# Kernel tuning notes

Measured on AMD Instinct MI355X. Metric: run time of the kernel, lower is better.

## Reference

```python
import jax, jax.numpy as jnp
import numpy as np

BS, SEQ, D = 8, 2048, 128
MASK_VALUE = -1000000.0


def setup_inputs() -> dict:
    key = jax.random.key(0)
    kq, kk, kv, kl = jax.random.split(key, 4)
    return {
        "queries": jax.random.normal(kq, (BS, SEQ, D), dtype=jnp.float32),
        "keys": jax.random.normal(kk, (BS, SEQ, D), dtype=jnp.float32),
        "values": jax.random.normal(kv, (BS, SEQ, D), dtype=jnp.float32),
        "valid_lens": jax.random.randint(kl, (BS,), 1, SEQ + 1, dtype=jnp.int32),
    }


def reference(queries, keys, values, valid_lens):
    d_k = keys.shape[-1]
    # (bs, seq_q, seq_k)
    scores = jnp.einsum("bqd,bkd->bqk", queries, keys) / jnp.sqrt(
        jnp.asarray(d_k, dtype=queries.dtype)
    )
    # padding mask over the LAST axis: position k valid iff k < valid_len[b]
    pos = jnp.arange(scores.shape[-1])  # (seq_k,)
    valid = pos[None, None, :] < valid_lens[:, None, None]  # (bs, 1, seq_k)
    scores = jnp.where(valid, scores, MASK_VALUE)
    attn = jax.nn.softmax(scores, axis=-1)
    # (bs, seq_q, d_v); dropout=0.0 -> identity
    return jnp.einsum("bqk,bkd->bqd", attn, values)
```

## Files before the change

### kernel.cpp

```cpp
#include <hip/hip_runtime.h>

typedef float f32x4 __attribute__((ext_vector_type(4)));
typedef short bf16x8 __attribute__((ext_vector_type(8)));
typedef short bf16x4 __attribute__((ext_vector_type(4)));
typedef unsigned int u32x2 __attribute__((ext_vector_type(2)));

#define BS    8
#define SEQ   2048
#define DH    128
#define BQ    32
#define BK    64
#define NT    256
#define CFIX  8.0f
#define SC2E  0.12751743f
#define NC2E  -11.541560327f

__device__ __forceinline__ unsigned short f2bf(float x) {
    unsigned u = __float_as_uint(x);
    u += 0x7FFFu + ((u >> 16) & 1u);
    return (unsigned short)(u >> 16);
}

__device__ __forceinline__ void gl_lds16(const unsigned short* g, unsigned short* l) {
    __builtin_amdgcn_global_load_lds(
        (const __attribute__((address_space(1))) unsigned int*)g,
        (__attribute__((address_space(3))) unsigned int*)l, 16, 0, 0);
}

__global__ __launch_bounds__(NT)
void conv_all(const float* __restrict__ K, const float* __restrict__ V,
              unsigned short* __restrict__ Kbf, unsigned short* __restrict__ Vt) {
    __shared__ unsigned short T[64][132];
    const int tid = threadIdx.x;
    const int bid = blockIdx.x;

    const int gtid = bid * NT + tid;
    #pragma unroll
    for (int i = 0; i < 8; ++i) {
        const int idx = i * (256 * NT) + gtid;
        float4 v = ((const float4*)K)[idx];
        ushort4 h;
        h.x = f2bf(v.x); h.y = f2bf(v.y); h.z = f2bf(v.z); h.w = f2bf(v.w);
        ((ushort4*)Kbf)[idx] = h;
    }

    const int vb = bid >> 5, s0 = (bid & 31) * 64;
    const float* Vb = V + ((size_t)vb * SEQ + s0) * DH;
    #pragma unroll
    for (int i = 0; i < 8; ++i) {
        const int row = i * 8 + (tid >> 5);
        const int col = (tid & 31) * 4;
        float4 v = *(const float4*)(Vb + (size_t)row * DH + col);
        ushort4 h;
        h.x = f2bf(v.x); h.y = f2bf(v.y); h.z = f2bf(v.z); h.w = f2bf(v.w);
        *(ushort4*)&T[row][col] = h;
    }
    __syncthreads();
    const int d = tid >> 1, sh = (tid & 1) * 32;
    unsigned short tmp[32] __attribute__((aligned(16)));
    #pragma unroll
    for (int s = 0; s < 32; ++s) tmp[s] = T[sh + s][d];
    unsigned short* dst = Vt + ((size_t)vb * DH + d) * SEQ + s0 + sh;
    #pragma unroll
    for (int g = 0; g < 4; ++g)
        *(uint4*)(dst + g * 8) = *(const uint4*)(tmp + g * 8);
}

__global__ __launch_bounds__(NT, 2)
void attn32(const float* __restrict__ Q, const unsigned short* __restrict__ Kbf,
            const unsigned short* __restrict__ Vt, const int* __restrict__ vlens,
            float* __restrict__ Out) {
    __shared__ unsigned short Ks[2][BK * DH];
    __shared__ unsigned short Vs[2][DH * BK];
    __shared__ float Lsc[2][32];

    const int tid  = threadIdx.x;
    const int wid  = tid >> 6, lane = tid & 63;
    const int quad = lane >> 4, l16 = lane & 15;
    const int qh   = wid >> 1, sh = wid & 1;
    const int bid  = blockIdx.x;
    const int b    = bid >> 6;
    const int q0   = (bid & 63) * BQ;
    const int vl   = vlens[b];

    const unsigned short* Kb  = Kbf + (size_t)b * SEQ * DH;
    const unsigned short* Vtb = Vt  + (size_t)b * DH * SEQ;

    bf16x8 qf[4];
    {
        const float* Qr = Q + ((size_t)b * SEQ + q0 + 16 * qh + l16) * DH;
        #pragma unroll
        for (int ks = 0; ks < 4; ++ks) {
            const float4 x = *(const float4*)(Qr + 32 * ks + 8 * quad);
            const float4 y = *(const float4*)(Qr + 32 * ks + 8 * quad + 4);
            unsigned short t8[8] __attribute__((aligned(16)));
            t8[0] = f2bf(x.x); t8[1] = f2bf(x.y); t8[2] = f2bf(x.z); t8[3] = f2bf(x.w);
            t8[4] = f2bf(y.x); t8[5] = f2bf(y.y); t8[6] = f2bf(y.z); t8[7] = f2bf(y.w);
            qf[ks] = *(const bf16x8*)t8;
        }
    }

    f32x4 o[8];
    #pragma unroll
    for (int n = 0; n < 8; ++n) o[n] = (f32x4){0.f, 0.f, 0.f, 0.f};
    float lsum = 0.f;

    const int ntiles = (vl + BK - 1) >> 6;

    auto stage = [&](int buf, int k0) {
        unsigned short* KsB = &Ks[buf][0];
        unsigned short* VsB = &Vs[buf][0];
        #pragma unroll
        for (int ii = 0; ii < 4; ++ii) {
            const int rb = 16 * wid + 4 * ii;
            const int r  = rb + (lane >> 4);
            const int c  = lane & 15;
            gl_lds16(Kb + (size_t)(k0 + r) * DH + ((c ^ (r & 15)) << 3),
                     KsB + (size_t)rb * DH);
        }
        #pragma unroll
        for (int jj = 0; jj < 4; ++jj) {
            const int db = 32 * wid + 8 * jj;
            const int d  = db + (lane >> 3);
            const int c  = lane & 7;
            gl_lds16(Vtb + (size_t)d * SEQ + k0 + ((c ^ (d & 7)) << 3),
                     VsB + (size_t)db * BK);
        }
    };

    stage(0, 0);

    for (int t = 0; t < ntiles; ++t) {
        const int k0 = t << 6;
        __syncthreads();
        if (t + 1 < ntiles) stage((t + 1) & 1, k0 + BK);

        const unsigned short* Kt  = &Ks[t & 1][0];
        const unsigned short* Vtl = &Vs[t & 1][0];

        f32x4 s2[2];
        s2[0] = (f32x4){0.f, 0.f, 0.f, 0.f};
        s2[1] = (f32x4){0.f, 0.f, 0.f, 0.f};
        __builtin_amdgcn_s_setprio(1);
        #pragma unroll
        for (int ks = 0; ks < 4; ++ks) {
            bf16x8 bk[2];
            #pragma unroll
            for (int nt = 0; nt < 2; ++nt)
                bk[nt] = *(const bf16x8*)(Kt + (size_t)(32 * sh + 16 * nt + l16) * DH +
                                          (((4 * ks + quad) ^ l16) << 3));
            #pragma unroll
            for (int nt = 0; nt < 2; ++nt)
                s2[nt] = __builtin_amdgcn_mfma_f32_16x16x32_bf16(bk[nt], qf[ks], s2[nt], 0, 0, 0);
        }
        __builtin_amdgcn_s_setprio(0);

        float p[2][4];
        if (k0 + BK <= vl) {
            #pragma unroll
            for (int nt = 0; nt < 2; ++nt)
                #pragma unroll
                for (int r = 0; r < 4; ++r) {
                    const float pv = __builtin_amdgcn_exp2f(fmaf(s2[nt][r], SC2E, NC2E));
                    p[nt][r] = pv;
                    lsum += pv;
                }
        } else {
            const int kb = k0 + 32 * sh + 4 * quad;
            #pragma unroll
            for (int nt = 0; nt < 2; ++nt)
                #pragma unroll
                for (int r = 0; r < 4; ++r) {
                    float pv = __builtin_amdgcn_exp2f(fmaf(s2[nt][r], SC2E, NC2E));
                    pv = (kb + 16 * nt + r < vl) ? pv : 0.0f;
                    p[nt][r] = pv;
                    lsum += pv;
                }
        }

        bf16x4 pa[2];
        #pragma unroll
        for (int nt = 0; nt < 2; ++nt) {
            unsigned w0, w1;
            asm("v_cvt_pk_bf16_f32 %0, %1, %2" : "=v"(w0) : "v"(p[nt][0]), "v"(p[nt][1]));
            asm("v_cvt_pk_bf16_f32 %0, %1, %2" : "=v"(w1) : "v"(p[nt][2]), "v"(p[nt][3]));
            u32x2 tw; tw.x = w0; tw.y = w1;
            pa[nt] = __builtin_bit_cast(bf16x4, tw);
        }

        __builtin_amdgcn_s_setprio(1);
        #pragma unroll
        for (int n = 0; n < 8; ++n) {
            const int dd = 16 * n + l16;
            #pragma unroll
            for (int nt = 0; nt < 2; ++nt) {
                const int g = 4 * sh + 2 * nt + (quad >> 1);
                const bf16x4 vb = *(const bf16x4*)(Vtl + (size_t)dd * BK +
                                        ((g ^ (dd & 7)) << 3) + ((quad & 1) << 2));
                o[n] = __builtin_amdgcn_mfma_f32_16x16x16bf16_1k(pa[nt], vb, o[n], 0, 0, 0);
            }
        }
        __builtin_amdgcn_s_setprio(0);
    }

    lsum += __shfl_xor(lsum, 16, 64);
    lsum += __shfl_xor(lsum, 32, 64);

    __syncthreads();
    float* Osc = (float*)&Ks[0][0];

    if (lane < 16) Lsc[sh][qh * 16 + l16] = lsum;
    if (sh == 0) {
        #pragma unroll
        for (int r = 0; r < 4; ++r) {
            float* dst = Osc + (size_t)qh * 2048 + (4 * quad + r) * 128 + l16;
            #pragma unroll
            for (int n = 0; n < 8; ++n) dst[16 * n] = o[n][r];
        }
    }
    __syncthreads();
    if (sh == 1) {
        #pragma unroll
        for (int r = 0; r < 4; ++r) {
            const float ls = Lsc[0][qh * 16 + 4 * quad + r] +
                             Lsc[1][qh * 16 + 4 * quad + r];
            const float inv = 1.0f / ls;
            const float* src = Osc + (size_t)qh * 2048 + (4 * quad + r) * 128 + l16;
            float* Or = Out + ((size_t)b * SEQ + q0 + 16 * qh + 4 * quad + r) * DH + l16;
            #pragma unroll
            for (int n = 0; n < 8; ++n)
                Or[16 * n] = (o[n][r] + src[16 * n]) * inv;
        }
    }
}

#define FBQ 32
#define QSTRIDE (DH + 4)
#define PSTRIDE (BK + 4)
__global__ __launch_bounds__(NT, 2)
void attn_fwd(const float* __restrict__ Q, const float* __restrict__ K,
              const float* __restrict__ V, const int* __restrict__ vlens,
              float* __restrict__ Out) {
    __shared__ float Qs[FBQ][QSTRIDE];
    __shared__ float KVs[BK][QSTRIDE];
    __shared__ float Ps[FBQ][PSTRIDE];
    __shared__ float l_s[FBQ];
    const int tid = threadIdx.x;
    const int b = blockIdx.y, q0 = blockIdx.x * FBQ;
    const int vl = vlens[b];
    const float scale = 0.088388347648318441f;
    const float* Qb = Q + ((size_t)b * SEQ + q0) * DH;
    const float* Kb = K + (size_t)b * SEQ * DH;
    const float* Vb = V + (size_t)b * SEQ * DH;
    {
        const int r = tid >> 5, c4 = (tid & 31) * 4;
        #pragma unroll
        for (int i = 0; i < 4; ++i)
            *(float4*)&Qs[i * 8 + r][c4] = *(const float4*)(Qb + (size_t)(i * 8 + r) * DH + c4);
    }
    const int sty = tid >> 4, stx = tid & 15;
    const int brow = tid >> 3, bpart = tid & 7;
    const int prg = tid >> 5, pcg = tid & 31;
    float lacc = 0.0f;
    float O[4][4];
    #pragma unroll
    for (int i = 0; i < 4; ++i)
        #pragma unroll
        for (int j = 0; j < 4; ++j) O[i][j] = 0.0f;
    const int ntiles = (vl + BK - 1) / BK;
    for (int t = 0; t < ntiles; ++t) {
        const int k0 = t * BK;
        __syncthreads();
        {
            const int r = tid >> 5, c4 = (tid & 31) * 4;
            #pragma unroll
            for (int i = 0; i < 8; ++i)
                *(float4*)&KVs[i * 8 + r][c4] = *(const float4*)(Kb + (size_t)(k0 + i * 8 + r) * DH + c4);
        }
        __syncthreads();
        float s0[4] = {0.f, 0.f, 0.f, 0.f}, s1[4] = {0.f, 0.f, 0.f, 0.f};
        #pragma unroll 2
        for (int d = 0; d < DH; d += 4) {
            const float4 qa = *(const float4*)&Qs[2 * sty][d];
            const float4 qb = *(const float4*)&Qs[2 * sty + 1][d];
            #pragma unroll
            for (int j = 0; j < 4; ++j) {
                const float4 kk = *(const float4*)&KVs[4 * stx + j][d];
                s0[j] += qa.x * kk.x + qa.y * kk.y + qa.z * kk.z + qa.w * kk.w;
                s1[j] += qb.x * kk.x + qb.y * kk.y + qb.z * kk.z + qb.w * kk.w;
            }
        }
        #pragma unroll
        for (int j = 0; j < 4; ++j) {
            const int kk = k0 + 4 * stx + j;
            const bool valid = kk < vl;
            Ps[2 * sty][4 * stx + j]     = valid ? __expf(s0[j] * scale - CFIX) : 0.f;
            Ps[2 * sty + 1][4 * stx + j] = valid ? __expf(s1[j] * scale - CFIX) : 0.f;
        }
        __syncthreads();
        {
            float ps = 0.f;
            #pragma unroll
            for (int i = 0; i < 8; ++i) ps += Ps[brow][bpart * 8 + i];
            #pragma unroll
            for (int off = 1; off < 8; off <<= 1) ps += __shfl_xor(ps, off, 64);
            if (bpart == 0) lacc += ps;
        }
        {
            const int r = tid >> 5, c4 = (tid & 31) * 4;
            float4 vreg[8];
            #pragma unroll
            for (int i = 0; i < 8; ++i)
                vreg[i] = *(const float4*)(Vb + (size_t)(k0 + i * 8 + r) * DH + c4);
            __syncthreads();
            #pragma unroll
            for (int i = 0; i < 8; ++i) *(float4*)&KVs[i * 8 + r][c4] = vreg[i];
        }
        __syncthreads();
        for (int k = 0; k < BK; k += 4) {
            float4 pr[4];
            #pragma unroll
            for (int i = 0; i < 4; ++i) pr[i] = *(const float4*)&Ps[prg * 4 + i][k];
            #pragma unroll
            for (int k2 = 0; k2 < 4; ++k2) {
                const float4 vv = *(const float4*)&KVs[k + k2][pcg * 4];
                #pragma unroll
                for (int i = 0; i < 4; ++i) {
                    const float p = ((const float*)&pr[i])[k2];
                    O[i][0] += p * vv.x; O[i][1] += p * vv.y;
                    O[i][2] += p * vv.z; O[i][3] += p * vv.w;
                }
            }
        }
    }
    if (bpart == 0) l_s[brow] = lacc;
    __syncthreads();
    float* Ob = Out + ((size_t)b * SEQ + q0) * DH;
    #pragma unroll
    for (int i = 0; i < 4; ++i) {
        const int row = prg * 4 + i;
        const float inv = 1.0f / l_s[row];
        float4 ov;
        ov.x = O[i][0] * inv; ov.y = O[i][1] * inv;
        ov.z = O[i][2] * inv; ov.w = O[i][3] * inv;
        *(float4*)(Ob + (size_t)row * DH + pcg * 4) = ov;
    }
}

extern "C" void kernel_launch(void* const* d_in, const int* in_sizes, int n_in,
                              void* d_out, int out_size, void* d_ws, size_t ws_size,
                              hipStream_t stream) {
    const float* Q = (const float*)d_in[0];
    const float* K = (const float*)d_in[1];
    const float* V = (const float*)d_in[2];
    const int* vlens = (const int*)d_in[3];
    float* Out = (float*)d_out;

    const size_t n = (size_t)BS * SEQ * DH;
    const size_t need = 2 * n * 2;

    if (ws_size >= need) {
        unsigned short* Kbf = (unsigned short*)d_ws;
        unsigned short* Vt  = Kbf + n;
        conv_all<<<dim3(256), dim3(NT), 0, stream>>>(K, V, Kbf, Vt);
        attn32<<<dim3(BS * (SEQ / BQ)), dim3(NT), 0, stream>>>(Q, Kbf, Vt, vlens, Out);
    } else {
        attn_fwd<<<dim3(SEQ / FBQ, BS), dim3(NT), 0, stream>>>(Q, K, V, vlens, Out);
    }
}
```

Before: 110.3 us.

## Halve attention tiles to 16 queries, split head dim across waves, pre-convert Q

The attention kernel now uses 16-query, 32-key tiles, giving 1024 blocks instead of 512. The four waves are split two ways on key halves and two ways on head-dim halves. Q is converted to bf16 in the prep kernel, so the attention kernel loads bf16 fragments directly, and the occupancy hint rises to 4 blocks per CU. The goal is better load balance and occupancy across CUs with variable valid lengths. The cost is twice as many K/V tile loads per query, smaller MFMA work per barrier, and an extra Q conversion pass through memory.

```diff
diff --git a/kernel.cpp b/kernel.cpp
--- a/kernel.cpp
+++ b/kernel.cpp
@@ -8,8 +8,8 @@
 #define BS    8
 #define SEQ   2048
 #define DH    128
-#define BQ    32
-#define BK    64
+#define BQ    16
+#define BK    32
 #define NT    256
 #define CFIX  8.0f
 #define SC2E  0.12751743f
@@ -28,8 +28,10 @@
 }
 
 __global__ __launch_bounds__(NT)
-void conv_all(const float* __restrict__ K, const float* __restrict__ V,
-              unsigned short* __restrict__ Kbf, unsigned short* __restrict__ Vt) {
+void conv_all(const float* __restrict__ Q, const float* __restrict__ K,
+              const float* __restrict__ V,
+              unsigned short* __restrict__ Qbf, unsigned short* __restrict__ Kbf,
+              unsigned short* __restrict__ Vt) {
     __shared__ unsigned short T[64][132];
     const int tid = threadIdx.x;
     const int bid = blockIdx.x;
@@ -38,10 +40,13 @@
     #pragma unroll
     for (int i = 0; i < 8; ++i) {
         const int idx = i * (256 * NT) + gtid;
-        float4 v = ((const float4*)K)[idx];
-        ushort4 h;
-        h.x = f2bf(v.x); h.y = f2bf(v.y); h.z = f2bf(v.z); h.w = f2bf(v.w);
-        ((ushort4*)Kbf)[idx] = h;
+        float4 k4 = ((const float4*)K)[idx];
+        float4 q4 = ((const float4*)Q)[idx];
+        ushort4 hk, hq;
+        hk.x = f2bf(k4.x); hk.y = f2bf(k4.y); hk.z = f2bf(k4.z); hk.w = f2bf(k4.w);
+        hq.x = f2bf(q4.x); hq.y = f2bf(q4.y); hq.z = f2bf(q4.z); hq.w = f2bf(q4.w);
+        ((ushort4*)Kbf)[idx] = hk;
+        ((ushort4*)Qbf)[idx] = hq;
     }
 
     const int vb = bid >> 5, s0 = (bid & 31) * 64;
@@ -66,21 +71,21 @@
         *(uint4*)(dst + g * 8) = *(const uint4*)(tmp + g * 8);
 }
 
-__global__ __launch_bounds__(NT, 2)
-void attn32(const float* __restrict__ Q, const unsigned short* __restrict__ Kbf,
+__global__ __launch_bounds__(NT, 4)
+void attn16(const unsigned short* __restrict__ Qbf, const unsigned short* __restrict__ Kbf,
             const unsigned short* __restrict__ Vt, const int* __restrict__ vlens,
             float* __restrict__ Out) {
     __shared__ unsigned short Ks[2][BK * DH];
     __shared__ unsigned short Vs[2][DH * BK];
-    __shared__ float Lsc[2][32];
+    __shared__ float Lsc[2][16];
 
     const int tid  = threadIdx.x;
     const int wid  = tid >> 6, lane = tid & 63;
     const int quad = lane >> 4, l16 = lane & 15;
-    const int qh   = wid >> 1, sh = wid & 1;
+    const int dh   = wid >> 1, sh = wid & 1;
     const int bid  = blockIdx.x;
-    const int b    = bid >> 6;
-    const int q0   = (bid & 63) * BQ;
+    const int b    = bid >> 7;
+    const int q0   = (bid & 127) * BQ;
     const int vl   = vlens[b];
 
     const unsigned short* Kb  = Kbf + (size_t)b * SEQ * DH;
@@ -88,42 +93,36 @@
 
     bf16x8 qf[4];
     {
-        const float* Qr = Q + ((size_t)b * SEQ + q0 + 16 * qh + l16) * DH;
-        #pragma unroll
-        for (int ks = 0; ks < 4; ++ks) {
-            const float4 x = *(const float4*)(Qr + 32 * ks + 8 * quad);
-            const float4 y = *(const float4*)(Qr + 32 * ks + 8 * quad + 4);
-            unsigned short t8[8] __attribute__((aligned(16)));
-            t8[0] = f2bf(x.x); t8[1] = f2bf(x.y); t8[2] = f2bf(x.z); t8[3] = f2bf(x.w);
-            t8[4] = f2bf(y.x); t8[5] = f2bf(y.y); t8[6] = f2bf(y.z); t8[7] = f2bf(y.w);
-            qf[ks] = *(const bf16x8*)t8;
-        }
-    }
-
-    f32x4 o[8];
-    #pragma unroll
-    for (int n = 0; n < 8; ++n) o[n] = (f32x4){0.f, 0.f, 0.f, 0.f};
+        const unsigned short* Qr = Qbf + ((size_t)b * SEQ + q0 + l16) * DH;
+        #pragma unroll
+        for (int ks = 0; ks < 4; ++ks)
+            qf[ks] = *(const bf16x8*)(Qr + 32 * ks + 8 * quad);
+    }
+
+    f32x4 o[4];
+    #pragma unroll
+    for (int n = 0; n < 4; ++n) o[n] = (f32x4){0.f, 0.f, 0.f, 0.f};
     float lsum = 0.f;
 
-    const int ntiles = (vl + BK - 1) >> 6;
+    const int ntiles = (vl + BK - 1) >> 5;
 
     auto stage = [&](int buf, int k0) {
         unsigned short* KsB = &Ks[buf][0];
         unsigned short* VsB = &Vs[buf][0];
         #pragma unroll
-        for (int ii = 0; ii < 4; ++ii) {
-            const int rb = 16 * wid + 4 * ii;
+        for (int ii = 0; ii < 2; ++ii) {
+            const int rb = 8 * wid + 4 * ii;
             const int r  = rb + (lane >> 4);
             const int c  = lane & 15;
             gl_lds16(Kb + (size_t)(k0 + r) * DH + ((c ^ (r & 15)) << 3),
                      KsB + (size_t)rb * DH);
         }
         #pragma unroll
-        for (int jj = 0; jj < 4; ++jj) {
-            const int db = 32 * wid + 8 * jj;
-            const int d  = db + (lane >> 3);
-            const int c  = lane & 7;
-            gl_lds16(Vtb + (size_t)d * SEQ + k0 + ((c ^ (d & 7)) << 3),
+        for (int jj = 0; jj < 2; ++jj) {
+            const int db = 32 * wid + 16 * jj;
+            const int d  = db + (lane >> 2);
+            const int c  = lane & 3;
+            gl_lds16(Vtb + (size_t)d * SEQ + k0 + ((c ^ (d & 3)) << 3),
                      VsB + (size_t)db * BK);
         }
     };
@@ -131,74 +130,59 @@
     stage(0, 0);
 
     for (int t = 0; t < ntiles; ++t) {
-        const int k0 = t << 6;
+        const int k0 = t << 5;
         __syncthreads();
         if (t + 1 < ntiles) stage((t + 1) & 1, k0 + BK);
 
         const unsigned short* Kt  = &Ks[t & 1][0];
         const unsigned short* Vtl = &Vs[t & 1][0];
 
-        f32x4 s2[2];
-        s2[0] = (f32x4){0.f, 0.f, 0.f, 0.f};
-        s2[1] = (f32x4){0.f, 0.f, 0.f, 0.f};
+        f32x4 s2 = (f32x4){0.f, 0.f, 0.f, 0.f};
         __builtin_amdgcn_s_setprio(1);
         #pragma unroll
         for (int ks = 0; ks < 4; ++ks) {
-            bf16x8 bk[2];
-            #pragma unroll
-            for (int nt = 0; nt < 2; ++nt)
-                bk[nt] = *(const bf16x8*)(Kt + (size_t)(32 * sh + 16 * nt + l16) * DH +
-                                          (((4 * ks + quad) ^ l16) << 3));
-            #pragma unroll
-            for (int nt = 0; nt < 2; ++nt)
-                s2[nt] = __builtin_amdgcn_mfma_f32_16x16x32_bf16(bk[nt], qf[ks], s2[nt], 0, 0, 0);
+            const bf16x8 bk = *(const bf16x8*)(Kt + (size_t)(16 * sh + l16) * DH +
+                                               (((4 * ks + quad) ^ l16) << 3));
+            s2 = __builtin_amdgcn_mfma_f32_16x16x32_bf16(bk, qf[ks], s2, 0, 0, 0);
         }
         __builtin_amdgcn_s_setprio(0);
 
-        float p[2][4];
+        float p[4];
         if (k0 + BK <= vl) {
             #pragma unroll
-            for (int nt = 0; nt < 2; ++nt)
-                #pragma unroll
-                for (int r = 0; r < 4; ++r) {
-                    const float pv = __builtin_amdgcn_exp2f(fmaf(s2[nt][r], SC2E, NC2E));
-                    p[nt][r] = pv;
-                    lsum += pv;
-                }
+            for (int r = 0; r < 4; ++r) {
+                const float pv = __builtin_amdgcn_exp2f(fmaf(s2[r], SC2E, NC2E));
+                p[r] = pv;
+                lsum += pv;
+            }
         } else {
-            const int kb = k0 + 32 * sh + 4 * quad;
-            #pragma unroll
-            for (int nt = 0; nt < 2; ++nt)
-                #pragma unroll
-                for (int r = 0; r < 4; ++r) {
-                    float pv = __builtin_amdgcn_exp2f(fmaf(s2[nt][r], SC2E, NC2E));
-                    pv = (kb + 16 * nt + r < vl) ? pv : 0.0f;
-                    p[nt][r] = pv;
-                    lsum += pv;
-                }
-        }
-
-        bf16x4 pa[2];
-        #pragma unroll
-        for (int nt = 0; nt < 2; ++nt) {
+            const int kb = k0 + 16 * sh + 4 * quad;
+            #pragma unroll
+            for (int r = 0; r < 4; ++r) {
+                float pv = __builtin_amdgcn_exp2f(fmaf(s2[r], SC2E, NC2E));
+                pv = (kb + r < vl) ? pv : 0.0f;
+                p[r] = pv;
+                lsum += pv;
+            }
+        }
+
+        bf16x4 pa;
+        {
             unsigned w0, w1;
-            asm("v_cvt_pk_bf16_f32 %0, %1, %2" : "=v"(w0) : "v"(p[nt][0]), "v"(p[nt][1]));
-            asm("v_cvt_pk_bf16_f32 %0, %1, %2" : "=v"(w1) : "v"(p[nt][2]), "v"(p[nt][3]));
+            asm("v_cvt_pk_bf16_f32 %0, %1, %2" : "=v"(w0) : "v"(p[0]), "v"(p[1]));
+            asm("v_cvt_pk_bf16_f32 %0, %1, %2" : "=v"(w1) : "v"(p[2]), "v"(p[3]));
             u32x2 tw; tw.x = w0; tw.y = w1;
-            pa[nt] = __builtin_bit_cast(bf16x4, tw);
+            pa = __builtin_bit_cast(bf16x4, tw);
         }
 
         __builtin_amdgcn_s_setprio(1);
         #pragma unroll
-        for (int n = 0; n < 8; ++n) {
-            const int dd = 16 * n + l16;
-            #pragma unroll
-            for (int nt = 0; nt < 2; ++nt) {
-                const int g = 4 * sh + 2 * nt + (quad >> 1);
-                const bf16x4 vb = *(const bf16x4*)(Vtl + (size_t)dd * BK +
-                                        ((g ^ (dd & 7)) << 3) + ((quad & 1) << 2));
-                o[n] = __builtin_amdgcn_mfma_f32_16x16x16bf16_1k(pa[nt], vb, o[n], 0, 0, 0);
-            }
+        for (int n = 0; n < 4; ++n) {
+            const int d = 64 * dh + 16 * n + l16;
+            const int c = 2 * sh + (quad >> 1);
+            const bf16x4 vb = *(const bf16x4*)(Vtl + (size_t)d * BK +
+                                    ((c ^ (d & 3)) << 3) + ((quad & 1) << 2));
+            o[n] = __builtin_amdgcn_mfma_f32_16x16x16bf16_1k(pa, vb, o[n], 0, 0, 0);
         }
         __builtin_amdgcn_s_setprio(0);
     }
@@ -209,40 +193,41 @@
     __syncthreads();
     float* Osc = (float*)&Ks[0][0];
 
-    if (lane < 16) Lsc[sh][qh * 16 + l16] = lsum;
+    if (dh == 0 && lane < 16) Lsc[sh][l16] = lsum;
     if (sh == 0) {
         #pragma unroll
-        for (int r = 0; r < 4; ++r) {
-            float* dst = Osc + (size_t)qh * 2048 + (4 * quad + r) * 128 + l16;
-            #pragma unroll
-            for (int n = 0; n < 8; ++n) dst[16 * n] = o[n][r];
-        }
+        for (int n = 0; n < 4; ++n)
+            #pragma unroll
+            for (int r = 0; r < 4; ++r)
+                Osc[((size_t)dh * 16 + 4 * quad + r) * 64 + 16 * n + l16] = o[n][r];
     }
     __syncthreads();
     if (sh == 1) {
         #pragma unroll
         for (int r = 0; r < 4; ++r) {
-            const float ls = Lsc[0][qh * 16 + 4 * quad + r] +
-                             Lsc[1][qh * 16 + 4 * quad + r];
+            const int row = 4 * quad + r;
+            const float ls = Lsc[0][row] + Lsc[1][row];
             const float inv = 1.0f / ls;
-            const float* src = Osc + (size_t)qh * 2048 + (4 * quad + r) * 128 + l16;
-            float* Or = Out + ((size_t)b * SEQ + q0 + 16 * qh + 4 * quad + r) * DH + l16;
-            #pragma unroll
-            for (int n = 0; n < 8; ++n)
-                Or[16 * n] = (o[n][r] + src[16 * n]) * inv;
+            #pragma unroll
+            for (int n = 0; n < 4; ++n) {
+                const float val = (o[n][r] +
+                    Osc[((size_t)dh * 16 + row) * 64 + 16 * n + l16]) * inv;
+                Out[((size_t)b * SEQ + q0 + row) * DH + 64 * dh + 16 * n + l16] = val;
+            }
         }
     }
 }
 
 #define FBQ 32
+#define FBK 64
 #define QSTRIDE (DH + 4)
-#define PSTRIDE (BK + 4)
+#define PSTRIDE (FBK + 4)
 __global__ __launch_bounds__(NT, 2)
 void attn_fwd(const float* __restrict__ Q, const float* __restrict__ K,
               const float* __restrict__ V, const int* __restrict__ vlens,
               float* __restrict__ Out) {
     __shared__ float Qs[FBQ][QSTRIDE];
-    __shared__ float KVs[BK][QSTRIDE];
+    __shared__ float KVs[FBK][QSTRIDE];
     __shared__ float Ps[FBQ][PSTRIDE];
     __shared__ float l_s[FBQ];
     const int tid = threadIdx.x;
@@ -266,10 +251,10 @@
     #pragma unroll
     for (int i = 0; i < 4; ++i)
         #pragma unroll
-        for (int j = 0; j < 4; ++j) O[i][j] = 0.0f;
-    const int ntiles = (vl + BK - 1) / BK;
+        for (int jj = 0; jj < 4; ++jj) O[i][jj] = 0.0f;
+    const int ntiles = (vl + FBK - 1) / FBK;
     for (int t = 0; t < ntiles; ++t) {
-        const int k0 = t * BK;
+        const int k0 = t * FBK;
         __syncthreads();
         {
             const int r = tid >> 5, c4 = (tid & 31) * 4;
@@ -284,18 +269,18 @@
             const float4 qa = *(const float4*)&Qs[2 * sty][d];
             const float4 qb = *(const float4*)&Qs[2 * sty + 1][d];
             #pragma unroll
-            for (int j = 0; j < 4; ++j) {
-                const float4 kk = *(const float4*)&KVs[4 * stx + j][d];
-                s0[j] += qa.x * kk.x + qa.y * kk.y + qa.z * kk.z + qa.w * kk.w;
-                s1[j] += qb.x * kk.x + qb.y * kk.y + qb.z * kk.z + qb.w * kk.w;
-            }
-        }
-        #pragma unroll
-        for (int j = 0; j < 4; ++j) {
-            const int kk = k0 + 4 * stx + j;
+            for (int jj = 0; jj < 4; ++jj) {
+                const float4 kk = *(const float4*)&KVs[4 * stx + jj][d];
+                s0[jj] += qa.x * kk.x + qa.y * kk.y + qa.z * kk.z + qa.w * kk.w;
+                s1[jj] += qb.x * kk.x + qb.y * kk.y + qb.z * kk.z + qb.w * kk.w;
+            }
+        }
+        #pragma unroll
+        for (int jj = 0; jj < 4; ++jj) {
+            const int kk = k0 + 4 * stx + jj;
             const bool valid = kk < vl;
-            Ps[2 * sty][4 * stx + j]     = valid ? __expf(s0[j] * scale - CFIX) : 0.f;
-            Ps[2 * sty + 1][4 * stx + j] = valid ? __expf(s1[j] * scale - CFIX) : 0.f;
+            Ps[2 * sty][4 * stx + jj]     = valid ? __expf(s0[jj] * scale - CFIX) : 0.f;
+            Ps[2 * sty + 1][4 * stx + jj] = valid ? __expf(s1[jj] * scale - CFIX) : 0.f;
         }
         __syncthreads();
         {
@@ -317,7 +302,7 @@
             for (int i = 0; i < 8; ++i) *(float4*)&KVs[i * 8 + r][c4] = vreg[i];
         }
         __syncthreads();
-        for (int k = 0; k < BK; k += 4) {
+        for (int k = 0; k < FBK; k += 4) {
             float4 pr[4];
             #pragma unroll
             for (int i = 0; i < 4; ++i) pr[i] = *(const float4*)&Ps[prg * 4 + i][k];
@@ -357,13 +342,14 @@
     float* Out = (float*)d_out;
 
     const size_t n = (size_t)BS * SEQ * DH;
-    const size_t need = 2 * n * 2;
+    const size_t need = 3 * n * 2;
 
     if (ws_size >= need) {
         unsigned short* Kbf = (unsigned short*)d_ws;
         unsigned short* Vt  = Kbf + n;
-        conv_all<<<dim3(256), dim3(NT), 0, stream>>>(K, V, Kbf, Vt);
-        attn32<<<dim3(BS * (SEQ / BQ)), dim3(NT), 0, stream>>>(Q, Kbf, Vt, vlens, Out);
+        unsigned short* Qbf = Vt + n;
+        conv_all<<<dim3(256), dim3(NT), 0, stream>>>(Q, K, V, Qbf, Kbf, Vt);
+        attn16<<<dim3(BS * (SEQ / BQ)), dim3(NT), 0, stream>>>(Qbf, Kbf, Vt, vlens, Out);
     } else {
         attn_fwd<<<dim3(SEQ / FBQ, BS), dim3(NT), 0, stream>>>(Q, K, V, vlens, Out);
     }
```

Measured after the change: 129.0 us. 16.9% more time.
